# Kernel optimization log

Measured on AMD Instinct MI355X. Metric: run time of the kernel, lower is better.

## Reference

```python
import jax, jax.numpy as jnp
import numpy as np


def setup_inputs() -> dict:
    key = jax.random.key(0)
    k1, k2 = jax.random.split(key)
    z = jax.random.normal(k1, (16, 256, 64, 64), dtype=jnp.float32)  # (t, latent_dim, H, W)
    emb = jax.random.normal(k2, (1024, 256), dtype=jnp.float32)      # (n_codes, latent_dim)
    return {"z": z, "emb": emb}


def reference(z, emb):
    # z: (t, a, b, c) with a == latent_dim; emb: (n_codes, a)
    t, a, b, c = z.shape
    # rearrange 't a b c -> t (b c) a'
    x = z.reshape(t, a, b * c).transpose(0, 2, 1)  # (t, bc, a)
    x2 = jnp.sum(x * x, axis=-1, keepdims=True)          # (t, bc, 1)
    e2 = jnp.sum(emb * emb, axis=-1)                     # (n_codes,)
    d2 = x2 + e2 - 2.0 * jnp.einsum('tna,ka->tnk', x, emb)  # (t, bc, n_codes)
    codes = jnp.argmin(d2, axis=-1)                      # (t, bc)
    return codes.reshape(t, b, c)
```

## Files before the change

### kernel.cpp

```cpp
#include <hip/hip_runtime.h>
#include <hip/hip_bf16.h>

#define TPB 512
#define NCODES 1024
#define DIMS 256
#define PIXB 64
#define DELTA 3.0f
#define CAP 16

typedef __attribute__((ext_vector_type(8))) short bf16x8;
typedef __attribute__((ext_vector_type(4))) float f32x4;

__device__ __forceinline__ void gll16(const void* g, void* l) {
    __builtin_amdgcn_global_load_lds(
        (const __attribute__((address_space(1))) void*)g,
        (__attribute__((address_space(3))) void*)l, 16, 0, 0);
}

__global__ __launch_bounds__(256) void prep_kernel(const float* __restrict__ emb,
                                                   ushort* __restrict__ eb,
                                                   float* __restrict__ e2) {
    const int w = threadIdx.x >> 6;
    const int l = threadIdx.x & 63;
    const int c = blockIdx.x * 4 + w;
    float4 v = *(const float4*)(emb + (size_t)c * DIMS + 4 * l);
    __hip_bfloat16 h0 = __float2bfloat16(v.x), h1 = __float2bfloat16(v.y);
    __hip_bfloat16 h2 = __float2bfloat16(v.z), h3 = __float2bfloat16(v.w);
    ushort4 u;
    u.x = *(ushort*)&h0; u.y = *(ushort*)&h1; u.z = *(ushort*)&h2; u.w = *(ushort*)&h3;
    const int st = (c >> 8) * 8 + (l >> 3);
    const int w8 = (c >> 5) & 7;
    const int cl = c & 31;
    const int j  = (l >> 1) & 3;
    const int e  = (4 * l) & 7;
    *(ushort4*)(eb + (((size_t)(st * 8 + w8) << 10) + (j << 8) + cl * 8 + e)) = u;
    float sq = v.x * v.x + v.y * v.y + v.z * v.z + v.w * v.w;
#pragma unroll
    for (int off = 1; off < 64; off <<= 1) sq += __shfl_xor(sq, off);
    if (l == 0) e2[c] = sq;
}

__global__ __launch_bounds__(TPB, 3) void vq_kernel(const float* __restrict__ z,
                                                    const float* __restrict__ emb,
                                                    const ushort* __restrict__ eb,
                                                    const float* __restrict__ e2g,
                                                    int* __restrict__ out) {
    __shared__ __align__(16) ushort xs2[32 * 64 * 8];
    __shared__ __align__(16) char pool[16384];

    float* const wmin   = (float*)pool;
    float* const minval = (float*)(pool + 2048);
    int*   const cnt    = (int*)(pool + 2304);
    int*   const cand   = (int*)(pool + 2560);
    float* const scand  = (float*)(pool + 6656);

    const int tid = threadIdx.x;
    const int w   = tid >> 6;
    const int L   = tid & 63;
    const int col = L & 15;
    const int q   = L >> 4;
    const int pixbase = blockIdx.x * PIXB;
    const int t  = pixbase >> 12;
    const int n0 = pixbase & 4095;

    const float* zbase = z + (((size_t)t * DIMS) << 12) + n0;

#define STAGE_Z(r_, h_) do {                                                      \
        const float* _src = zbase                                                 \
            + ((size_t)((r_) * 32 + w * 4 + (L >> 4)) << 12) + ((L & 15) << 2);   \
        char* _dst = pool + (h_) * 8192 + (w << 10);                              \
        gll16(_src, _dst);                                                        \
    } while (0)

#define CONVERT(r_, h_) do {                                                      \
        const float* _zs = (const float*)(pool + (h_) * 8192) + (w << 8);         \
        float _a0 = _zs[L];                                                       \
        float _a1 = _zs[64 + L];                                                  \
        float _a2 = _zs[128 + L];                                                 \
        float _a3 = _zs[192 + L];                                                 \
        __hip_bfloat16 _h0 = __float2bfloat16(_a0);                               \
        __hip_bfloat16 _h1 = __float2bfloat16(_a1);                               \
        __hip_bfloat16 _h2 = __float2bfloat16(_a2);                               \
        __hip_bfloat16 _h3 = __float2bfloat16(_a3);                               \
        ushort4 _u;                                                               \
        _u.x = *(ushort*)&_h0; _u.y = *(ushort*)&_h1;                             \
        _u.z = *(ushort*)&_h2; _u.w = *(ushort*)&_h3;                             \
        const int _g = (r_) * 4 + (w >> 1);                                       \
        *(ushort4*)&xs2[(size_t)((_g * 64 + L) * 8 + ((w & 1) << 2))] = _u;       \
    } while (0)

    STAGE_Z(0, 0);
    STAGE_Z(1, 1);
    asm volatile("s_waitcnt vmcnt(1)" ::: "memory");
    CONVERT(0, 0);
    asm volatile("s_waitcnt lgkmcnt(0)" ::: "memory");
    STAGE_Z(2, 0);
    asm volatile("s_waitcnt vmcnt(1)" ::: "memory");
    CONVERT(1, 1);
    asm volatile("s_waitcnt lgkmcnt(0)" ::: "memory");
    STAGE_Z(3, 1);
    asm volatile("s_waitcnt vmcnt(1)" ::: "memory");
    CONVERT(2, 0);
    asm volatile("s_waitcnt lgkmcnt(0)" ::: "memory");
    STAGE_Z(4, 0);
    asm volatile("s_waitcnt vmcnt(1)" ::: "memory");
    CONVERT(3, 1);
    asm volatile("s_waitcnt lgkmcnt(0)" ::: "memory");
    STAGE_Z(5, 1);
    asm volatile("s_waitcnt vmcnt(1)" ::: "memory");
    CONVERT(4, 0);
    asm volatile("s_waitcnt lgkmcnt(0)" ::: "memory");
    STAGE_Z(6, 0);
    asm volatile("s_waitcnt vmcnt(1)" ::: "memory");
    CONVERT(5, 1);
    asm volatile("s_waitcnt lgkmcnt(0)" ::: "memory");
    STAGE_Z(7, 1);
    asm volatile("s_waitcnt vmcnt(1)" ::: "memory");
    CONVERT(6, 0);
    asm volatile("s_waitcnt lgkmcnt(0)" ::: "memory");
    asm volatile("s_waitcnt vmcnt(0)" ::: "memory");
    CONVERT(7, 1);

#define LOADT(a0_, a1_, st_) do {                                                 \
        const ushort* _et = eb + (((size_t)((st_) * 8 + w)) << 10)                \
                               + (q << 8) + (col << 3);                           \
        a0_ = *(const bf16x8*)_et;                                                \
        a1_ = *(const bf16x8*)(_et + 128);                                        \
    } while (0)

    bf16x8 pf[2][2];
    LOADT(pf[0][0], pf[0][1], 0);
    LOADT(pf[1][0], pf[1][1], 1);

    __syncthreads();
    if (tid < 64) { minval[tid] = 3.4e38f; cnt[tid] = 0; }

#pragma unroll 1
    for (int cc = 0; cc < 4; ++cc) {
        f32x4 acc[2][4];
#pragma unroll
        for (int mt = 0; mt < 2; ++mt)
#pragma unroll
            for (int nt = 0; nt < 4; ++nt) acc[mt][nt] = (f32x4){0.f, 0.f, 0.f, 0.f};

#pragma unroll
        for (int kc = 0; kc < 8; ++kc) {
            const int s = cc * 8 + kc;
            bf16x8 a0 = pf[kc & 1][0];
            bf16x8 a1 = pf[kc & 1][1];
            bf16x8 bfr[4];
#pragma unroll
            for (int nt = 0; nt < 4; ++nt)
                bfr[nt] = *(const bf16x8*)&xs2[(size_t)(((kc * 4 + q) * 64 + nt * 16 + col) * 8)];
            {
                const int st = (s + 2 < 31) ? s + 2 : 31;
                LOADT(pf[kc & 1][0], pf[kc & 1][1], st);
            }
            __builtin_amdgcn_s_setprio(1);
#pragma unroll
            for (int nt = 0; nt < 4; ++nt)
                acc[0][nt] = __builtin_amdgcn_mfma_f32_16x16x32_bf16(
                    a0, bfr[nt], acc[0][nt], 0, 0, 0);
#pragma unroll
            for (int nt = 0; nt < 4; ++nt)
                acc[1][nt] = __builtin_amdgcn_mfma_f32_16x16x32_bf16(
                    a1, bfr[nt], acc[1][nt], 0, 0, 0);
            __builtin_amdgcn_s_setprio(0);
        }

        f32x4 e4[2];
#pragma unroll
        for (int mt = 0; mt < 2; ++mt)
            e4[mt] = *(const f32x4*)(e2g + cc * 256 + w * 32 + mt * 16 + q * 4);

#pragma unroll
        for (int nt = 0; nt < 4; ++nt) {
            float m = 3.4e38f;
#pragma unroll
            for (int mt = 0; mt < 2; ++mt)
#pragma unroll
                for (int r = 0; r < 4; ++r) {
                    float s = e4[mt][r] - 2.f * acc[mt][nt][r];
                    m = fminf(m, s);
                }
            m = fminf(m, __shfl_xor(m, 16));
            m = fminf(m, __shfl_xor(m, 32));
            wmin[w * 64 + nt * 16 + col] = m;
        }
        __syncthreads();
        if (tid < 64) {
            float m = minval[tid];
#pragma unroll
            for (int ww = 0; ww < 8; ++ww) m = fminf(m, wmin[ww * 64 + tid]);
            minval[tid] = m;
        }
        __syncthreads();
#pragma unroll
        for (int nt = 0; nt < 4; ++nt) {
            const int px = nt * 16 + col;
            const float thr = minval[px] + DELTA;
#pragma unroll
            for (int mt = 0; mt < 2; ++mt)
#pragma unroll
                for (int r = 0; r < 4; ++r) {
                    float s = e4[mt][r] - 2.f * acc[mt][nt][r];
                    if (s <= thr) {
                        int pos = atomicAdd(&cnt[px], 1);
                        if (pos < CAP) {
                            cand[px * CAP + pos]  = cc * 256 + w * 32 + mt * 16 + q * 4 + r;
                            scand[px * CAP + pos] = s;
                        }
                    }
                }
        }
    }
    __syncthreads();

#pragma unroll 1
    for (int pi = 0; pi < 8; ++pi) {
        const int px = w * 8 + pi;
        const int n  = cnt[px];
        if (n <= CAP) {
            const float thr = minval[px] + DELTA;
            bool surv = (L < n) && (scand[px * CAP + L] <= thr);
            unsigned long long mask = __ballot(surv);
            if (__popcll(mask) == 1) {
                if (L == 0) out[pixbase + px] = cand[px * CAP + (__ffsll(mask) - 1)];
                continue;
            }
            const float* zp = z + (((size_t)t * DIMS + 4 * L) << 12) + n0 + px;
            float x0 = zp[0];
            float x1 = zp[(size_t)1 << 12];
            float x2 = zp[(size_t)2 << 12];
            float x3 = zp[(size_t)3 << 12];
            float bs = 3.4e38f;
            int   bi = 0;
            unsigned long long mm = mask;
            while (mm) {
                int k = __ffsll(mm) - 1; mm &= mm - 1;
                int c = cand[px * CAP + k];
                float4 ev = *(const float4*)(emb + (size_t)c * DIMS + 4 * L);
                float p = x0 * ev.x + x1 * ev.y + x2 * ev.z + x3 * ev.w;
#pragma unroll
                for (int off = 1; off < 64; off <<= 1) p += __shfl_xor(p, off);
                float s = e2g[c] - 2.f * p;
                if (s < bs || (s == bs && c < bi)) { bs = s; bi = c; }
            }
            if (L == 0) out[pixbase + px] = bi;
        } else {
            const float* zp = z + (((size_t)t * DIMS + 4 * L) << 12) + n0 + px;
            float x0 = zp[0];
            float x1 = zp[(size_t)1 << 12];
            float x2 = zp[(size_t)2 << 12];
            float x3 = zp[(size_t)3 << 12];
            float bs = 3.4e38f;
            int   bi = 0;
            for (int c = 0; c < NCODES; ++c) {
                float4 ev = *(const float4*)(emb + (size_t)c * DIMS + 4 * L);
                float p = x0 * ev.x + x1 * ev.y + x2 * ev.z + x3 * ev.w;
#pragma unroll
                for (int off = 1; off < 64; off <<= 1) p += __shfl_xor(p, off);
                float s = e2g[c] - 2.f * p;
                if (s < bs || (s == bs && c < bi)) { bs = s; bi = c; }
            }
            if (L == 0) out[pixbase + px] = bi;
        }
    }
#undef STAGE_Z
#undef CONVERT
#undef LOADT
}

extern "C" void kernel_launch(void* const* d_in, const int* in_sizes, int n_in,
                              void* d_out, int out_size, void* d_ws, size_t ws_size,
                              hipStream_t stream) {
    const float* z   = (const float*)d_in[0];
    const float* emb = (const float*)d_in[1];
    int* out = (int*)d_out;

    ushort* eb = (ushort*)d_ws;
    float*  e2 = (float*)((char*)d_ws + (size_t)NCODES * DIMS * sizeof(ushort));

    prep_kernel<<<256, 256, 0, stream>>>(emb, eb, e2);
    vq_kernel<<<(16 * 64 * 64) / PIXB, TPB, 0, stream>>>(z, emb, eb, e2, out);
}
```

Measured before the change: 156.9 us.

## Shrink LDS pool to single-buffered z staging to fit four blocks per CU

Removes the double buffer for z staging and shrinks the candidate capacity from 16 to 10, cutting the shared pool from 16KB to 8KB. Launch bounds now request 4 blocks per CU instead of 3, aiming for higher occupancy to hide latency. In exchange, each z load is now fully serialized with its conversion (wait for vmcnt(0) every round), so that overlap is lost. The smaller candidate cap also raises the chance of overflowing to the slow fallback path.

```diff
diff --git a/kernel.cpp b/kernel.cpp
--- a/kernel.cpp
+++ b/kernel.cpp
@@ -6,7 +6,7 @@
 #define DIMS 256
 #define PIXB 64
 #define DELTA 3.0f
-#define CAP 16
+#define CAP 10
 
 typedef __attribute__((ext_vector_type(8))) short bf16x8;
 typedef __attribute__((ext_vector_type(4))) float f32x4;
@@ -40,19 +40,19 @@
     if (l == 0) e2[c] = sq;
 }
 
-__global__ __launch_bounds__(TPB, 3) void vq_kernel(const float* __restrict__ z,
+__global__ __launch_bounds__(TPB, 4) void vq_kernel(const float* __restrict__ z,
                                                     const float* __restrict__ emb,
                                                     const ushort* __restrict__ eb,
                                                     const float* __restrict__ e2g,
                                                     int* __restrict__ out) {
     __shared__ __align__(16) ushort xs2[32 * 64 * 8];
-    __shared__ __align__(16) char pool[16384];
+    __shared__ __align__(16) char pool[8192];
 
     float* const wmin   = (float*)pool;
     float* const minval = (float*)(pool + 2048);
     int*   const cnt    = (int*)(pool + 2304);
     int*   const cand   = (int*)(pool + 2560);
-    float* const scand  = (float*)(pool + 6656);
+    float* const scand  = (float*)(pool + 5120);
 
     const int tid = threadIdx.x;
     const int w   = tid >> 6;
@@ -65,15 +65,15 @@
 
     const float* zbase = z + (((size_t)t * DIMS) << 12) + n0;
 
-#define STAGE_Z(r_, h_) do {                                                      \
+#define STAGE_Z(r_) do {                                                          \
         const float* _src = zbase                                                 \
             + ((size_t)((r_) * 32 + w * 4 + (L >> 4)) << 12) + ((L & 15) << 2);   \
-        char* _dst = pool + (h_) * 8192 + (w << 10);                              \
+        char* _dst = pool + (w << 10);                                            \
         gll16(_src, _dst);                                                        \
     } while (0)
 
-#define CONVERT(r_, h_) do {                                                      \
-        const float* _zs = (const float*)(pool + (h_) * 8192) + (w << 8);         \
+#define CONVERT(r_) do {                                                          \
+        const float* _zs = (const float*)pool + (w << 8);                         \
         float _a0 = _zs[L];                                                       \
         float _a1 = _zs[64 + L];                                                  \
         float _a2 = _zs[128 + L];                                                 \
@@ -89,37 +89,15 @@
         *(ushort4*)&xs2[(size_t)((_g * 64 + L) * 8 + ((w & 1) << 2))] = _u;       \
     } while (0)
 
-    STAGE_Z(0, 0);
-    STAGE_Z(1, 1);
-    asm volatile("s_waitcnt vmcnt(1)" ::: "memory");
-    CONVERT(0, 0);
-    asm volatile("s_waitcnt lgkmcnt(0)" ::: "memory");
-    STAGE_Z(2, 0);
-    asm volatile("s_waitcnt vmcnt(1)" ::: "memory");
-    CONVERT(1, 1);
-    asm volatile("s_waitcnt lgkmcnt(0)" ::: "memory");
-    STAGE_Z(3, 1);
-    asm volatile("s_waitcnt vmcnt(1)" ::: "memory");
-    CONVERT(2, 0);
-    asm volatile("s_waitcnt lgkmcnt(0)" ::: "memory");
-    STAGE_Z(4, 0);
-    asm volatile("s_waitcnt vmcnt(1)" ::: "memory");
-    CONVERT(3, 1);
-    asm volatile("s_waitcnt lgkmcnt(0)" ::: "memory");
-    STAGE_Z(5, 1);
-    asm volatile("s_waitcnt vmcnt(1)" ::: "memory");
-    CONVERT(4, 0);
-    asm volatile("s_waitcnt lgkmcnt(0)" ::: "memory");
-    STAGE_Z(6, 0);
-    asm volatile("s_waitcnt vmcnt(1)" ::: "memory");
-    CONVERT(5, 1);
-    asm volatile("s_waitcnt lgkmcnt(0)" ::: "memory");
-    STAGE_Z(7, 1);
-    asm volatile("s_waitcnt vmcnt(1)" ::: "memory");
-    CONVERT(6, 0);
-    asm volatile("s_waitcnt lgkmcnt(0)" ::: "memory");
-    asm volatile("s_waitcnt vmcnt(0)" ::: "memory");
-    CONVERT(7, 1);
+#define ZROUND(r_) do {                                                           \
+        STAGE_Z(r_);                                                              \
+        asm volatile("s_waitcnt vmcnt(0)" ::: "memory");                          \
+        CONVERT(r_);                                                              \
+        asm volatile("s_waitcnt lgkmcnt(0)" ::: "memory");                        \
+    } while (0)
+
+    ZROUND(0); ZROUND(1); ZROUND(2); ZROUND(3);
+    ZROUND(4); ZROUND(5); ZROUND(6); ZROUND(7);
 
 #define LOADT(a0_, a1_, st_) do {                                                 \
         const ushort* _et = eb + (((size_t)((st_) * 8 + w)) << 10)                \
@@ -268,6 +246,7 @@
     }
 #undef STAGE_Z
 #undef CONVERT
+#undef ZROUND
 #undef LOADT
 }
 
```

Measured after the change: 570.0 us. +263.2%, slower.
